# Kernel optimization log

Measured on AMD Instinct MI355X. Metric: run time of the kernel, lower is better.

The kernel has to match this reference:

```python
import jax, jax.numpy as jnp
import numpy as np

NUM_HEADS = 16
LN_EPS = 1e-5


def setup_inputs() -> dict:
    key = jax.random.key(0)
    ks = jax.random.split(key, 6)
    b, s, d = 2, 2048, 1024
    scale = 1.0 / np.sqrt(d)
    return {
        "x": jax.random.normal(ks[0], (b, s, d), dtype=jnp.float32),
        "W_w": jax.random.normal(ks[1], (3 * d, d), dtype=jnp.float32) * scale,
        "W_b": jax.random.normal(ks[2], (3 * d,), dtype=jnp.float32) * 0.01,
        "proj_w": jax.random.normal(ks[3], (d, d), dtype=jnp.float32) * scale,
        "proj_b": jax.random.normal(ks[4], (d,), dtype=jnp.float32) * 0.01,
        "gamma": jnp.ones((d,), dtype=jnp.float32),
        "beta": jnp.zeros((d,), dtype=jnp.float32),
    }


def reference(x, W_w, W_b, proj_w, proj_b, gamma, beta):
    b, s, d = x.shape
    h = NUM_HEADS
    hd = d // h
    # fused QKV projection: [b,s,3d]
    qkv = x @ W_w.T + W_b
    q, k, v = jnp.split(qkv, 3, axis=-1)
    # [b,s,d] -> [b,h,s,hd]
    q, k, v = (z.reshape(b, s, h, hd).transpose(0, 2, 1, 3) for z in (q, k, v))
    # NOTE: original scales by sqrt(d), not sqrt(head_dim)
    attn = jnp.einsum('bhqd,bhkd->bhqk', q, k) / jnp.sqrt(jnp.asarray(d, x.dtype))
    attn_weights = jax.nn.softmax(attn, axis=-1)  # [b,h,s,s]
    o = jnp.einsum('bhqk,bhkd->bhqd', attn_weights, v)
    o = o.transpose(0, 2, 1, 3).reshape(b, s, d)
    out = o @ proj_w.T + proj_b  # dropout is identity at eval
    y = x + out
    mu = jnp.mean(y, axis=-1, keepdims=True)
    var = jnp.var(y, axis=-1, keepdims=True)
    y_norm = (y - mu) / jnp.sqrt(var + LN_EPS) * gamma + beta
    return (y_norm, attn_weights)
```

## Files before the change

### kernel.cpp

```cpp
#include <hip/hip_runtime.h>
#include <cstdint>

#define BB 2
#define SS 2048
#define DD 1024
#define HH 16
#define HDIM 64
#define MM (BB*SS)
#define N3 (3*DD)

typedef __attribute__((ext_vector_type(4))) float f32x4;
typedef __attribute__((ext_vector_type(8))) __bf16 bf16x8;

static __device__ __forceinline__ unsigned short f2bf_fast(float f) {
  __bf16 h = (__bf16)f;
  return __builtin_bit_cast(unsigned short, h);
}

static __device__ __forceinline__ uint4 pack8f(const float4 a, const float4 b) {
  union { unsigned short us[8]; uint4 v; } pk;
  pk.us[0] = f2bf_fast(a.x); pk.us[1] = f2bf_fast(a.y); pk.us[2] = f2bf_fast(a.z); pk.us[3] = f2bf_fast(a.w);
  pk.us[4] = f2bf_fast(b.x); pk.us[5] = f2bf_fast(b.y); pk.us[6] = f2bf_fast(b.z); pk.us[7] = f2bf_fast(b.w);
  return pk.v;
}

static __device__ __forceinline__ void gload16(const unsigned short* g, unsigned short* l) {
  __builtin_amdgcn_global_load_lds(
      (const __attribute__((address_space(1))) void*)g,
      (__attribute__((address_space(3))) void*)l, 16, 0, 0);
}

__global__ __launch_bounds__(256) void cvt_kernel(
    const float* __restrict__ x, const float* __restrict__ Ww,
    const float* __restrict__ pw,
    unsigned short* __restrict__ xb, unsigned short* __restrict__ Wwb,
    unsigned short* __restrict__ pwb) {
  const size_t i = ((size_t)blockIdx.x * 256 + threadIdx.x) * 8;
  const float* src;
  unsigned short* dst;
  if (i < 4194304u)       { src = x  + i;            dst = xb  + i; }
  else if (i < 7340032u)  { src = Ww + (i - 4194304u); dst = Wwb + (i - 4194304u); }
  else                    { src = pw + (i - 7340032u); dst = pwb + (i - 7340032u); }
  const float4* s4 = (const float4*)src;
  *(uint4*)dst = pack8f(s4[0], s4[1]);
}

__global__ __launch_bounds__(256) void gemm_qkv(
    const unsigned short* __restrict__ xb, const unsigned short* __restrict__ Wwb,
    const float* __restrict__ Wb,
    unsigned short* __restrict__ qb, unsigned short* __restrict__ kb,
    unsigned short* __restrict__ vbT) {
  __shared__ __align__(16) unsigned short Sh[128 * 132];
  unsigned short* As0 = Sh;
  unsigned short* As1 = Sh + 4096;
  unsigned short* Bs0 = Sh + 8192;
  unsigned short* Bs1 = Sh + 12288;
  const int t = threadIdx.x;
  const int l = t & 63, w = t >> 6;
  const int wr = w >> 1, wc = w & 1;
  const int m0 = blockIdx.y * 128, n0 = blockIdx.x * 128;
  f32x4 acc[4][4] = {};

  for (int kt = 0; kt < DD; kt += 64) {
    __syncthreads();
    #pragma unroll
    for (int i = 0; i < 2; ++i) {
      const int row = (i * 4 + w) * 16 + (l >> 2);
      const int cc = (l & 3) * 8;
      gload16(xb  + (size_t)(m0 + row) * DD + kt + cc,      &As0[(i * 4 + w) * 512]);
      gload16(xb  + (size_t)(m0 + row) * DD + kt + 32 + cc, &As1[(i * 4 + w) * 512]);
      gload16(Wwb + (size_t)(n0 + row) * DD + kt + cc,      &Bs0[(i * 4 + w) * 512]);
      gload16(Wwb + (size_t)(n0 + row) * DD + kt + 32 + cc, &Bs1[(i * 4 + w) * 512]);
    }
    __syncthreads();
    #pragma unroll
    for (int ks = 0; ks < 2; ++ks) {
      const unsigned short* As = ks ? As1 : As0;
      const unsigned short* Bs = ks ? Bs1 : Bs0;
      bf16x8 a[4], b[4];
      #pragma unroll
      for (int i = 0; i < 4; ++i) {
        a[i] = __builtin_bit_cast(bf16x8, *(const uint4*)&As[(wr * 64 + i * 16 + (l & 15)) * 32 + (l >> 4) * 8]);
        b[i] = __builtin_bit_cast(bf16x8, *(const uint4*)&Bs[(wc * 64 + i * 16 + (l & 15)) * 32 + (l >> 4) * 8]);
      }
      #pragma unroll
      for (int i = 0; i < 4; ++i)
        #pragma unroll
        for (int j = 0; j < 4; ++j)
          acc[i][j] = __builtin_amdgcn_mfma_f32_16x16x32_bf16(a[i], b[j], acc[i][j], 0, 0, 0);
    }
  }
  __syncthreads();

  if (n0 < 2048) {
    const bool isq = (n0 < 1024);
    #pragma unroll
    for (int i = 0; i < 4; ++i)
      #pragma unroll
      for (int j = 0; j < 4; ++j)
        #pragma unroll
        for (int r = 0; r < 4; ++r) {
          const int row = m0 + wr * 64 + i * 16 + (l >> 4) * 4 + r;
          const int col = n0 + wc * 64 + j * 16 + (l & 15);
          const float v = acc[i][j][r] + Wb[col];
          const int bidx = row >> 11, srow = row & 2047;
          const int cc = col & 1023, head = cc >> 6, hd = cc & 63;
          const size_t idx = ((size_t)((bidx * HH + head) * SS + srow)) * HDIM + hd;
          if (isq) qb[idx] = f2bf_fast(v * 0.04508422f);
          else     kb[idx] = f2bf_fast(v);
        }
  } else {
    unsigned short* Tt = Sh;
    #pragma unroll
    for (int i = 0; i < 4; ++i)
      #pragma unroll
      for (int j = 0; j < 4; ++j)
        #pragma unroll
        for (int r = 0; r < 4; ++r) {
          const int rr = wr * 64 + i * 16 + (l >> 4) * 4 + r;
          const int cl = wc * 64 + j * 16 + (l & 15);
          Tt[rr * 132 + cl] = f2bf_fast(acc[i][j][r] + Wb[n0 + cl]);
        }
    __syncthreads();
    const int bidx = m0 >> 11, srow0 = m0 & 2047;
    const int q = t & 3;
    #pragma unroll
    for (int ci = 0; ci < 2; ++ci) {
      const int c = ci * 64 + (t >> 2);
      const int vcol = n0 - 2048 + c;
      const int head = vcol >> 6, hd = vcol & 63;
      unsigned short* dst = vbT + ((size_t)(bidx * HH + head) * HDIM + hd) * SS + srow0;
      #pragma unroll
      for (int e8 = 0; e8 < 4; ++e8) {
        const int r0 = e8 * 32 + q * 8;
        union { unsigned short us[8]; uint4 v; } pk;
        #pragma unroll
        for (int e = 0; e < 8; ++e) pk.us[e] = Tt[(r0 + e) * 132 + c];
        *(uint4*)(dst + r0) = pk.v;
      }
    }
  }
}

__global__ __launch_bounds__(256) void attn_kernel(
    const unsigned short* __restrict__ qb,
    const unsigned short* __restrict__ kb,
    const unsigned short* __restrict__ vbT,
    unsigned short* __restrict__ ob,
    float* __restrict__ attn_out) {
  __shared__ float Ored[4][64][68];
  __shared__ float Lred[4][64];
  const int t = threadIdx.x;
  const int l = t & 63, w = t >> 6;
  const int q_l = l & 15, hi = l >> 4;
  const int bid = blockIdx.x;
  const int swz = (bid & 7) * 128 + (bid >> 3);
  const int bh = swz >> 5;
  const int q0 = (swz & 31) * 64;
  const size_t base = (size_t)bh * SS * HDIM;

  bf16x8 qa[4][2];
  #pragma unroll
  for (int j = 0; j < 4; ++j)
    #pragma unroll
    for (int kc = 0; kc < 2; ++kc)
      qa[j][kc] = __builtin_bit_cast(bf16x8,
          *(const uint4*)(qb + base + (size_t)(q0 + j * 16 + q_l) * HDIM + kc * 32 + hi * 8));

  const unsigned short* kga = kb + base + (size_t)(w * 16 + q_l) * HDIM + hi * 8;
  const unsigned short* vga = vbT + ((size_t)bh * HDIM + q_l) * SS + w * 16 + hi * 4;

  float lsum[4] = {0.f, 0.f, 0.f, 0.f};
  {
    uint4 k0 = *(const uint4*)(kga);
    uint4 k1 = *(const uint4*)(kga + 32);
    for (int kt = 0; kt < SS; kt += 64) {
      const bool more = (kt + 64) < SS;
      uint4 n0, n1;
      if (more) {
        n0 = *(const uint4*)(kga + (size_t)(kt + 64) * HDIM);
        n1 = *(const uint4*)(kga + (size_t)(kt + 64) * HDIM + 32);
      }
      f32x4 sQ[4] = {};
      const bf16x8 kf0 = __builtin_bit_cast(bf16x8, k0);
      const bf16x8 kf1 = __builtin_bit_cast(bf16x8, k1);
      __builtin_amdgcn_s_setprio(1);
      #pragma unroll
      for (int j = 0; j < 4; ++j) {
        sQ[j] = __builtin_amdgcn_mfma_f32_16x16x32_bf16(kf0, qa[j][0], sQ[j], 0, 0, 0);
        sQ[j] = __builtin_amdgcn_mfma_f32_16x16x32_bf16(kf1, qa[j][1], sQ[j], 0, 0, 0);
      }
      __builtin_amdgcn_s_setprio(0);
      #pragma unroll
      for (int j = 0; j < 4; ++j)
        #pragma unroll
        for (int r = 0; r < 4; ++r)
          lsum[j] += __builtin_amdgcn_exp2f(sQ[j][r]);
      k0 = n0; k1 = n1;
    }
  }
  #pragma unroll
  for (int j = 0; j < 4; ++j) {
    float s = lsum[j];
    s += __shfl_xor(s, 16);
    s += __shfl_xor(s, 32);
    lsum[j] = s;
  }
  if (hi == 0) {
    #pragma unroll
    for (int j = 0; j < 4; ++j) Lred[w][j * 16 + q_l] = lsum[j];
  }
  __syncthreads();
  float rl[4];
  #pragma unroll
  for (int j = 0; j < 4; ++j)
    rl[j] = 1.0f / (Lred[0][j * 16 + q_l] + Lred[1][j * 16 + q_l] +
                    Lred[2][j * 16 + q_l] + Lred[3][j * 16 + q_l]);

  float* pbs[4];
  #pragma unroll
  for (int j = 0; j < 4; ++j)
    pbs[j] = attn_out + ((size_t)bh * SS + (q0 + j * 16 + q_l)) * SS + w * 16 + hi * 4;

  f32x4 of[4][4] = {};
  for (int kt = 0; kt < SS; kt += 128) {
    const uint4 k0 = *(const uint4*)(kga + (size_t)kt * HDIM);
    const uint4 k1 = *(const uint4*)(kga + (size_t)kt * HDIM + 32);
    const uint4 k2 = *(const uint4*)(kga + (size_t)(kt + 64) * HDIM);
    const uint4 k3 = *(const uint4*)(kga + (size_t)(kt + 64) * HDIM + 32);
    uint2 vv0[4], vv1[4];
    #pragma unroll
    for (int d4 = 0; d4 < 4; ++d4) {
      vv0[d4] = *(const uint2*)(vga + (size_t)(d4 * 16) * SS + kt);
      vv1[d4] = *(const uint2*)(vga + (size_t)(d4 * 16) * SS + kt + 64);
    }
    const bf16x8 kf0 = __builtin_bit_cast(bf16x8, k0);
    const bf16x8 kf1 = __builtin_bit_cast(bf16x8, k1);
    const bf16x8 kf2 = __builtin_bit_cast(bf16x8, k2);
    const bf16x8 kf3 = __builtin_bit_cast(bf16x8, k3);
    f32x4 sQa[4] = {}, sQb[4] = {};
    __builtin_amdgcn_s_setprio(1);
    #pragma unroll
    for (int j = 0; j < 4; ++j) {
      sQa[j] = __builtin_amdgcn_mfma_f32_16x16x32_bf16(kf0, qa[j][0], sQa[j], 0, 0, 0);
      sQa[j] = __builtin_amdgcn_mfma_f32_16x16x32_bf16(kf1, qa[j][1], sQa[j], 0, 0, 0);
      sQb[j] = __builtin_amdgcn_mfma_f32_16x16x32_bf16(kf2, qa[j][0], sQb[j], 0, 0, 0);
      sQb[j] = __builtin_amdgcn_mfma_f32_16x16x32_bf16(kf3, qa[j][1], sQb[j], 0, 0, 0);
    }
    __builtin_amdgcn_s_setprio(0);
    bf16x8 pbp[4];
    #pragma unroll
    for (int j = 0; j < 4; ++j) {
      float4 pva, pvb;
      pva.x = __builtin_amdgcn_exp2f(sQa[j][0]) * rl[j];
      pva.y = __builtin_amdgcn_exp2f(sQa[j][1]) * rl[j];
      pva.z = __builtin_amdgcn_exp2f(sQa[j][2]) * rl[j];
      pva.w = __builtin_amdgcn_exp2f(sQa[j][3]) * rl[j];
      pvb.x = __builtin_amdgcn_exp2f(sQb[j][0]) * rl[j];
      pvb.y = __builtin_amdgcn_exp2f(sQb[j][1]) * rl[j];
      pvb.z = __builtin_amdgcn_exp2f(sQb[j][2]) * rl[j];
      pvb.w = __builtin_amdgcn_exp2f(sQb[j][3]) * rl[j];
      __builtin_nontemporal_store(*(const f32x4*)&pva, (f32x4*)(pbs[j] + kt));
      __builtin_nontemporal_store(*(const f32x4*)&pvb, (f32x4*)(pbs[j] + kt + 64));
      pbp[j] = __builtin_bit_cast(bf16x8, pack8f(pva, pvb));
    }
    __builtin_amdgcn_s_setprio(1);
    #pragma unroll
    for (int d4 = 0; d4 < 4; ++d4) {
      uint4 vp; vp.x = vv0[d4].x; vp.y = vv0[d4].y; vp.z = vv1[d4].x; vp.w = vv1[d4].y;
      const bf16x8 vfp = __builtin_bit_cast(bf16x8, vp);
      #pragma unroll
      for (int j = 0; j < 4; ++j)
        of[d4][j] = __builtin_amdgcn_mfma_f32_16x16x32_bf16(vfp, pbp[j], of[d4][j], 0, 0, 0);
    }
    __builtin_amdgcn_s_setprio(0);
  }

  #pragma unroll
  for (int d4 = 0; d4 < 4; ++d4)
    #pragma unroll
    for (int j = 0; j < 4; ++j)
      *(f32x4*)&Ored[w][j * 16 + q_l][d4 * 16 + hi * 4] = of[d4][j];
  __syncthreads();
  const int bidx = bh >> 4, h_ = bh & 15;
  const int qf = w * 16 + q_l;
  union { unsigned short us[16]; uint4 v[2]; } opk;
  #pragma unroll
  for (int c4 = 0; c4 < 4; ++c4) {
    const int d0 = hi * 16 + c4 * 4;
    f32x4 s = *(const f32x4*)&Ored[0][qf][d0];
    s += *(const f32x4*)&Ored[1][qf][d0];
    s += *(const f32x4*)&Ored[2][qf][d0];
    s += *(const f32x4*)&Ored[3][qf][d0];
    opk.us[c4 * 4 + 0] = f2bf_fast(s[0]);
    opk.us[c4 * 4 + 1] = f2bf_fast(s[1]);
    opk.us[c4 * 4 + 2] = f2bf_fast(s[2]);
    opk.us[c4 * 4 + 3] = f2bf_fast(s[3]);
  }
  unsigned short* orow = ob + ((size_t)bidx * SS + (q0 + qf)) * DD + h_ * 64 + hi * 16;
  *(uint4*)orow = opk.v[0];
  *(uint4*)(orow + 8) = opk.v[1];
}

__global__ __launch_bounds__(256) void gemm_proj(
    const unsigned short* __restrict__ ob, const unsigned short* __restrict__ pwb,
    const float* __restrict__ pb, const float* __restrict__ x,
    float* __restrict__ y) {
  __shared__ __align__(16) unsigned short Ps[12288];
  unsigned short* As0 = Ps;
  unsigned short* As1 = Ps + 2048;
  unsigned short* Bs0 = Ps + 4096;
  unsigned short* Bs1 = Ps + 8192;
  const int t = threadIdx.x;
  const int l = t & 63, w = t >> 6;
  const int wr = w >> 1, wc = w & 1;
  const int m0 = blockIdx.y * 64, n0 = blockIdx.x * 128;
  f32x4 acc[2][4] = {};

  for (int kt = 0; kt < DD; kt += 64) {
    __syncthreads();
    {
      const int rowA = w * 16 + (l >> 2);
      const int cc = (l & 3) * 8;
      gload16(ob + (size_t)(m0 + rowA) * DD + kt + cc,      &As0[w * 512]);
      gload16(ob + (size_t)(m0 + rowA) * DD + kt + 32 + cc, &As1[w * 512]);
      #pragma unroll
      for (int i = 0; i < 2; ++i) {
        const int rowB = (i * 4 + w) * 16 + (l >> 2);
        gload16(pwb + (size_t)(n0 + rowB) * DD + kt + cc,      &Bs0[(i * 4 + w) * 512]);
        gload16(pwb + (size_t)(n0 + rowB) * DD + kt + 32 + cc, &Bs1[(i * 4 + w) * 512]);
      }
    }
    __syncthreads();
    #pragma unroll
    for (int ks = 0; ks < 2; ++ks) {
      const unsigned short* As = ks ? As1 : As0;
      const unsigned short* Bs = ks ? Bs1 : Bs0;
      bf16x8 a[2], b[4];
      #pragma unroll
      for (int i = 0; i < 2; ++i)
        a[i] = __builtin_bit_cast(bf16x8, *(const uint4*)&As[(wr * 32 + i * 16 + (l & 15)) * 32 + (l >> 4) * 8]);
      #pragma unroll
      for (int j = 0; j < 4; ++j)
        b[j] = __builtin_bit_cast(bf16x8, *(const uint4*)&Bs[(wc * 64 + j * 16 + (l & 15)) * 32 + (l >> 4) * 8]);
      #pragma unroll
      for (int i = 0; i < 2; ++i)
        #pragma unroll
        for (int j = 0; j < 4; ++j)
          acc[i][j] = __builtin_amdgcn_mfma_f32_16x16x32_bf16(a[i], b[j], acc[i][j], 0, 0, 0);
    }
  }
  #pragma unroll
  for (int i = 0; i < 2; ++i)
    #pragma unroll
    for (int j = 0; j < 4; ++j)
      #pragma unroll
      for (int r = 0; r < 4; ++r) {
        const int row = m0 + wr * 32 + i * 16 + (l >> 4) * 4 + r;
        const int col = n0 + wc * 64 + j * 16 + (l & 15);
        const size_t idx = (size_t)row * DD + col;
        y[idx] = acc[i][j][r] + pb[col] + x[idx];
      }
}

__global__ __launch_bounds__(256) void ln_kernel(
    float* __restrict__ y, const float* __restrict__ gamma,
    const float* __restrict__ beta) {
  const int row = blockIdx.x;
  const int t = threadIdx.x;
  const float4 v = ((const float4*)(y + (size_t)row * DD))[t];
  float s  = v.x + v.y + v.z + v.w;
  float s2 = v.x * v.x + v.y * v.y + v.z * v.z + v.w * v.w;
  #pragma unroll
  for (int off = 1; off < 64; off <<= 1) { s += __shfl_xor(s, off); s2 += __shfl_xor(s2, off); }
  __shared__ float red[8];
  const int l = t & 63, w = t >> 6;
  if (l == 0) { red[w] = s; red[4 + w] = s2; }
  __syncthreads();
  s  = red[0] + red[1] + red[2] + red[3];
  s2 = red[4] + red[5] + red[6] + red[7];
  const float mu = s * (1.0f / DD);
  const float var = s2 * (1.0f / DD) - mu * mu;
  const float rs = rsqrtf(var + 1e-5f);
  const float4 g  = ((const float4*)gamma)[t];
  const float4 be = ((const float4*)beta)[t];
  float4 o;
  o.x = (v.x - mu) * rs * g.x + be.x;
  o.y = (v.y - mu) * rs * g.y + be.y;
  o.z = (v.z - mu) * rs * g.z + be.z;
  o.w = (v.w - mu) * rs * g.w + be.w;
  ((float4*)(y + (size_t)row * DD))[t] = o;
}

extern "C" void kernel_launch(void* const* d_in, const int* in_sizes, int n_in,
                              void* d_out, int out_size, void* d_ws, size_t ws_size,
                              hipStream_t stream) {
  const float* x     = (const float*)d_in[0];
  const float* Ww    = (const float*)d_in[1];
  const float* Wb    = (const float*)d_in[2];
  const float* Pw    = (const float*)d_in[3];
  const float* Pb    = (const float*)d_in[4];
  const float* gamma = (const float*)d_in[5];
  const float* beta  = (const float*)d_in[6];

  float* out      = (float*)d_out;
  float* y_norm   = out;
  float* attn_out = out + (size_t)MM * DD;

  char* ws = (char*)d_ws;
  unsigned short* qb  = (unsigned short*)(ws);
  unsigned short* kb  = (unsigned short*)(ws +  8388608);
  unsigned short* vbT = (unsigned short*)(ws + 16777216);
  unsigned short* ob  = (unsigned short*)(ws + 25165824);
  unsigned short* xb  = (unsigned short*)(ws + 33554432);
  unsigned short* Wwb = (unsigned short*)(ws + 41943040);
  unsigned short* pwb = (unsigned short*)(ws + 48234496);

  cvt_kernel<<<4096, 256, 0, stream>>>(x, Ww, Pw, xb, Wwb, pwb);
  gemm_qkv<<<dim3(N3 / 128, MM / 128), 256, 0, stream>>>(xb, Wwb, Wb, qb, kb, vbT);
  attn_kernel<<<1024, 256, 0, stream>>>(qb, kb, vbT, ob, attn_out);
  gemm_proj<<<dim3(DD / 128, MM / 64), 256, 0, stream>>>(ob, pwb, Pb, x, y_norm);
  ln_kernel<<<MM, 256, 0, stream>>>(y_norm, gamma, beta);
}
```

Measured before the change: 242.4 us.

## Split attention row-sum pass into a separate kernel writing reciprocal sums

Moves the first pass, which computes softmax denominators, out of the attention kernel into its own kernel that writes reciprocal row sums to workspace. The attention kernel then reads these and only does the probability write and PV pass. The aim is to lower register and LDS pressure per kernel and so raise occupancy. The cost is an extra launch, a small global round trip for the sums, and reloading Q in both kernels. The sums buffer reuses the xb workspace region, which is safe only because xb is no longer read after the QKV GEMM.

```diff
diff --git a/kernel.cpp b/kernel.cpp
--- a/kernel.cpp
+++ b/kernel.cpp
@@ -142,13 +142,10 @@
   }
 }
 
-__global__ __launch_bounds__(256) void attn_kernel(
+__global__ __launch_bounds__(256) void lsum_kernel(
     const unsigned short* __restrict__ qb,
     const unsigned short* __restrict__ kb,
-    const unsigned short* __restrict__ vbT,
-    unsigned short* __restrict__ ob,
-    float* __restrict__ attn_out) {
-  __shared__ float Ored[4][64][68];
+    float* __restrict__ rls) {
   __shared__ float Lred[4][64];
   const int t = threadIdx.x;
   const int l = t & 63, w = t >> 6;
@@ -168,7 +165,6 @@
           *(const uint4*)(qb + base + (size_t)(q0 + j * 16 + q_l) * HDIM + kc * 32 + hi * 8));
 
   const unsigned short* kga = kb + base + (size_t)(w * 16 + q_l) * HDIM + hi * 8;
-  const unsigned short* vga = vbT + ((size_t)bh * HDIM + q_l) * SS + w * 16 + hi * 4;
 
   float lsum[4] = {0.f, 0.f, 0.f, 0.f};
   {
@@ -211,11 +207,48 @@
     for (int j = 0; j < 4; ++j) Lred[w][j * 16 + q_l] = lsum[j];
   }
   __syncthreads();
+  if (w == 0 && hi == 0) {
+    #pragma unroll
+    for (int j = 0; j < 4; ++j) {
+      const float tot = Lred[0][j * 16 + q_l] + Lred[1][j * 16 + q_l] +
+                        Lred[2][j * 16 + q_l] + Lred[3][j * 16 + q_l];
+      rls[(size_t)bh * SS + q0 + j * 16 + q_l] = 1.0f / tot;
+    }
+  }
+}
+
+__global__ __launch_bounds__(256) void attn_kernel(
+    const unsigned short* __restrict__ qb,
+    const unsigned short* __restrict__ kb,
+    const unsigned short* __restrict__ vbT,
+    const float* __restrict__ rls,
+    unsigned short* __restrict__ ob,
+    float* __restrict__ attn_out) {
+  __shared__ float Ored[4][64][68];
+  const int t = threadIdx.x;
+  const int l = t & 63, w = t >> 6;
+  const int q_l = l & 15, hi = l >> 4;
+  const int bid = blockIdx.x;
+  const int swz = (bid & 7) * 128 + (bid >> 3);
+  const int bh = swz >> 5;
+  const int q0 = (swz & 31) * 64;
+  const size_t base = (size_t)bh * SS * HDIM;
+
+  bf16x8 qa[4][2];
+  #pragma unroll
+  for (int j = 0; j < 4; ++j)
+    #pragma unroll
+    for (int kc = 0; kc < 2; ++kc)
+      qa[j][kc] = __builtin_bit_cast(bf16x8,
+          *(const uint4*)(qb + base + (size_t)(q0 + j * 16 + q_l) * HDIM + kc * 32 + hi * 8));
+
+  const unsigned short* kga = kb + base + (size_t)(w * 16 + q_l) * HDIM + hi * 8;
+  const unsigned short* vga = vbT + ((size_t)bh * HDIM + q_l) * SS + w * 16 + hi * 4;
+
   float rl[4];
   #pragma unroll
   for (int j = 0; j < 4; ++j)
-    rl[j] = 1.0f / (Lred[0][j * 16 + q_l] + Lred[1][j * 16 + q_l] +
-                    Lred[2][j * 16 + q_l] + Lred[3][j * 16 + q_l]);
+    rl[j] = rls[(size_t)bh * SS + q0 + j * 16 + q_l];
 
   float* pbs[4];
   #pragma unroll
@@ -415,10 +448,12 @@
   unsigned short* xb  = (unsigned short*)(ws + 33554432);
   unsigned short* Wwb = (unsigned short*)(ws + 41943040);
   unsigned short* pwb = (unsigned short*)(ws + 48234496);
+  float*          rls = (float*)(ws + 33554432);
 
   cvt_kernel<<<4096, 256, 0, stream>>>(x, Ww, Pw, xb, Wwb, pwb);
   gemm_qkv<<<dim3(N3 / 128, MM / 128), 256, 0, stream>>>(xb, Wwb, Wb, qb, kb, vbT);
-  attn_kernel<<<1024, 256, 0, stream>>>(qb, kb, vbT, ob, attn_out);
+  lsum_kernel<<<1024, 256, 0, stream>>>(qb, kb, rls);
+  attn_kernel<<<1024, 256, 0, stream>>>(qb, kb, vbT, rls, ob, attn_out);
   gemm_proj<<<dim3(DD / 128, MM / 64), 256, 0, stream>>>(ob, pwb, Pb, x, y_norm);
   ln_kernel<<<MM, 256, 0, stream>>>(y_norm, gamma, beta);
 }
```

Result: slower. 258.1 us (+6.5%).
